# Kernel optimization log

Measured on AMD Instinct MI355X. Metric: run time of the kernel, lower is better.

## Reference

```python
import jax, jax.numpy as jnp
import numpy as np

B, T, C, NH = 4, 827, 1024, 16
HS = C // NH
SCALE = 1.0 / float(np.sqrt(HS))


def setup_inputs() -> dict:
    key = jax.random.key(0)
    ks = jax.random.split(key, 16)
    d = {}
    d["x"] = jax.random.normal(ks[0], (B, T, C), jnp.float32)
    d["x_kv"] = jax.random.normal(ks[1], (B, T, C), jnp.float32)
    d["h"] = jax.random.normal(ks[2], (B, NH, T, T), jnp.float32) * 0.1
    for i, name in enumerate(["f01", "f02", "f12", "b01", "b02", "b12"]):
        d[name] = jax.random.uniform(ks[3 + i], (B, 256, 256), jnp.float32)
    for i, name in enumerate(["Wq", "Wk", "Wv", "Wp"]):
        d[name] = jax.random.normal(ks[9 + i], (C, C), jnp.float32) * 0.02
    for name in ["bq", "bk", "bv", "bp"]:
        d[name] = jnp.zeros((C,), jnp.float32)
    return d


def _sm(a):
    return jax.nn.softmax(a, axis=-1)


def reference(x, x_kv, h, f01, f02, f12, b01, b02, b12,
              Wq, bq, Wk, bk, Wv, bv, Wp, bp):
    Bb, Tt, Cc = x.shape

    def heads(t):  # [B,T,C] -> [B,NH,T,HS]
        return t.reshape(Bb, Tt, NH, HS).transpose(0, 2, 1, 3)

    q = heads(x @ Wq.T + bq)
    k = heads(x_kv @ Wk.T + bk)
    v = heads(x_kv @ Wv.T + bv)

    att = jnp.einsum('bhqd,bhkd->bhqk', q, k) * SCALE + h  # adaptive bias add

    # region-specific partial softmax (frame1->frame0, frame2->frame0, frame2->frame1)
    att = att.at[:, :, 285:541, 0:256].set(_sm(att[:, :, 285:541, 0:256]))
    att = att.at[:, :, 571:827, 0:256].set(_sm(att[:, :, 571:827, 0:256]))
    att = att.at[:, :, 571:827, 286:542].set(_sm(att[:, :, 571:827, 286:542]))

    # bidirectional epipolar maps (backward maps used transposed)
    b01t = b01.transpose(0, 2, 1)
    b02t = b02.transpose(0, 2, 1)
    b12t = b12.transpose(0, 2, 1)
    m12 = (f12 * b12t >= 0.1).astype(att.dtype)  # [B,256,256]

    # bi_epi_ratio (T==827 branch), computed BEFORE the multiplicative masking
    r3 = att[:, :, 571:827, 286:542]            # [B,NH,256,256]
    att_mean = r3.mean(-1)                       # [B,NH,256]
    att_mask_mean = (r3 * m12[:, None]).sum(-1) / m12.sum(-1)[:, None]
    bi_epi_ratio = att_mask_mean.mean(1) / att_mean.mean(1)  # [B,256]

    # att_for: forward-only masking (clone); att: forward*backward masking
    att_for = att
    att_for = att_for.at[:, :, 285:541, 0:256].multiply(f01[:, None])
    att_for = att_for.at[:, :, 571:827, 0:256].multiply(f02[:, None])
    att_for = att_for.at[:, :, 571:827, 286:542].multiply(f12[:, None])
    att = att.at[:, :, 285:541, 0:256].multiply((b01t * f01)[:, None])
    att = att.at[:, :, 571:827, 0:256].multiply((b02t * f02)[:, None])
    att = att.at[:, :, 571:827, 286:542].multiply((b12t * f12)[:, None])

    causal = jnp.tril(jnp.ones((Tt, Tt), dtype=bool))
    aw = jnp.where(causal, att, -jnp.inf)
    # re-softmax of the already masked+multiplied regions (overwrites, then global softmax)
    aw = aw.at[:, :, 571:827, 0:256].set(_sm(att[:, :, 571:827, 0:256]))
    aw = aw.at[:, :, 571:827, 286:542].set(_sm(att[:, :, 571:827, 286:542]))
    aw = _sm(aw)

    y = jnp.einsum('bhqk,bhkd->bhqd', aw, v)
    y = y.transpose(0, 2, 1, 3).reshape(Bb, Tt, Cc)
    y = y @ Wp.T + bp  # resid dropout is identity (pdrop=0 / eval)
    return y, bi_epi_ratio
```

## Files before the change

### kernel.cpp

```cpp
#include <hip/hip_runtime.h>
#include <cstdint>
#include <cstddef>

#define Tn  827
#define Cn  1024
#define BTn 3308
#define TPn 832
#define YSZ 3387392

typedef unsigned short u16;
typedef unsigned short u16x4 __attribute__((ext_vector_type(4)));
typedef __bf16 bf16_t;
typedef bf16_t bf16x8 __attribute__((ext_vector_type(8)));
typedef float f32x4 __attribute__((ext_vector_type(4)));

#define GLD(gp, lp) __builtin_amdgcn_global_load_lds( \
    (__attribute__((address_space(1))) void*)(gp),    \
    (__attribute__((address_space(3))) void*)(lp), 16, 0, 0)

__device__ inline u16 f32_to_bf16(float f) {
  union { float f; unsigned u; } v; v.f = f;
  unsigned u = v.u;
  u += 0x7fffu + ((u >> 16) & 1u);
  return (u16)(u >> 16);
}

__global__ __launch_bounds__(256)
void cvt_all_k(const float* __restrict__ x, const float* __restrict__ xkv,
               const float* __restrict__ wq, const float* __restrict__ wk,
               const float* __restrict__ wv, const float* __restrict__ wp,
               u16* __restrict__ xb, u16* __restrict__ xkb,
               u16* __restrict__ wqb, u16* __restrict__ wkb,
               u16* __restrict__ wvb, u16* __restrict__ wpb,
               u16* __restrict__ Vt)
{
  const long NX = 846848;
  const long NW = 262144;
  long qidx = (long)blockIdx.x * 256 + threadIdx.x;
  const float* s; u16* d; long base;
  if (qidx < NX)            { s = x;   d = xb;  base = qidx; }
  else if (qidx < 2 * NX)   { s = xkv; d = xkb; base = qidx - NX; }
  else {
    long w = qidx - 2 * NX;
    int wi = (int)(w / NW);
    if (wi >= 4) {
      long p = w - 4 * NW;
      if (p < 20480) {
        int row = (int)(p / 5);
        int col = 827 + (int)(p - (long)row * 5);
        Vt[(size_t)row * TPn + col] = 0;
      }
      return;
    }
    base = w - (long)wi * NW;
    if      (wi == 0) { s = wq; d = wqb; }
    else if (wi == 1) { s = wk; d = wkb; }
    else if (wi == 2) { s = wv; d = wvb; }
    else              { s = wp; d = wpb; }
  }
  const float4 v = *(const float4*)(s + base * 4);
  u16x4 o;
  o.x = f32_to_bf16(v.x); o.y = f32_to_bf16(v.y);
  o.z = f32_to_bf16(v.z); o.w = f32_to_bf16(v.w);
  *(u16x4*)(d + base * 4) = o;
}

__global__ __launch_bounds__(256)
void gemm_qkv_k(const u16* __restrict__ xb, const u16* __restrict__ xkb,
                const u16* __restrict__ wqb, const u16* __restrict__ wkb,
                const u16* __restrict__ wvb,
                const float* __restrict__ bq, const float* __restrict__ bk,
                const float* __restrict__ bv,
                u16* __restrict__ Qb, u16* __restrict__ Kb, u16* __restrict__ Vt)
{
  const int zz = blockIdx.z;
  const u16* A  = (zz == 0) ? xb : xkb;
  const u16* Bw = (zz == 0) ? wqb : (zz == 1) ? wkb : wvb;
  const float* bias = (zz == 0) ? bq : (zz == 1) ? bk : bv;

  const int tid  = threadIdx.x;
  const int lane = tid & 63;
  const int wave = tid >> 6;
  const int wm = wave >> 1, wn = wave & 1;
  const int m0 = blockIdx.x * 128;
  const int n0 = blockIdx.y * 128;

  __shared__ u16 As[2][4096];
  __shared__ u16 Bs[2][4096];

  f32x4 acc[4][4];
  const f32x4 zero4 = {0.f, 0.f, 0.f, 0.f};
  #pragma unroll
  for (int i = 0; i < 4; ++i)
    #pragma unroll
    for (int j = 0; j < 4; ++j)
      acc[i][j] = zero4;

#define QKV_STAGE(buf_, kt_) do {                                        \
    const int k0_ = (kt_) << 5;                                          \
    _Pragma("unroll")                                                    \
    for (int it = 0; it < 2; ++it) {                                     \
      const int cbase = it * 256 + wave * 64;                            \
      const int c  = cbase + lane;                                       \
      const int r_ = c >> 2;                                             \
      const int ko_ = (c & 3) << 3;                                      \
      if (m0 + r_ < BTn)                                                 \
        GLD(A  + (size_t)(m0 + r_) * Cn + k0_ + ko_, As[buf_] + cbase * 8); \
      GLD(Bw + (size_t)(n0 + r_) * Cn + k0_ + ko_, Bs[buf_] + cbase * 8);  \
    }                                                                    \
  } while (0)

  QKV_STAGE(0, 0);
  __syncthreads();

  for (int kt = 0; kt < 32; ++kt) {
    const int cur = kt & 1;
    if (kt < 31) QKV_STAGE(cur ^ 1, kt + 1);

    bf16x8 af[4], bfr[4];
    #pragma unroll
    for (int i = 0; i < 4; ++i) {
      const int r = wm * 64 + i * 16 + (lane & 15);
      af[i] = *(const bf16x8*)(As[cur] + r * 32 + ((lane >> 4) << 3));
    }
    #pragma unroll
    for (int j = 0; j < 4; ++j) {
      const int r = wn * 64 + j * 16 + (lane & 15);
      bfr[j] = *(const bf16x8*)(Bs[cur] + r * 32 + ((lane >> 4) << 3));
    }
    #pragma unroll
    for (int i = 0; i < 4; ++i)
      #pragma unroll
      for (int j = 0; j < 4; ++j)
        acc[i][j] = __builtin_amdgcn_mfma_f32_16x16x32_bf16(af[i], bfr[j], acc[i][j], 0, 0, 0);
    __syncthreads();
  }
#undef QKV_STAGE

  const int cq = lane >> 4, cl = lane & 15;
  if (zz < 2) {
    u16* D = (zz == 0) ? Qb : Kb;
    #pragma unroll
    for (int i = 0; i < 4; ++i) {
      #pragma unroll
      for (int j = 0; j < 4; ++j) {
        const int rb  = m0 + wm * 64 + i * 16 + cq * 4;
        const int col = n0 + wn * 64 + j * 16 + cl;
        const float bc = bias[col];
        #pragma unroll
        for (int r = 0; r < 4; ++r) {
          const int row = rb + r;
          if (row < BTn) D[(size_t)row * Cn + col] = f32_to_bf16(acc[i][j][r] + bc);
        }
      }
    }
  } else {
    #pragma unroll
    for (int j = 0; j < 4; ++j) {
      const int col = n0 + wn * 64 + j * 16 + cl;
      const int hh = col >> 6, dd = col & 63;
      const float bc = bias[col];
      #pragma unroll
      for (int i = 0; i < 4; ++i) {
        const int rb = m0 + wm * 64 + i * 16 + cq * 4;
        #pragma unroll
        for (int r = 0; r < 4; ++r) {
          const int row = rb + r;
          if (row < BTn) {
            const int bb = row / Tn;
            const int t  = row - bb * Tn;
            Vt[((size_t)((bb * 16 + hh) * 64 + dd)) * TPn + t] = f32_to_bf16(acc[i][j][r] + bc);
          }
        }
      }
    }
  }
}

template<int BM, int BN, int MODE>
__global__ __launch_bounds__(256)
void gemm_k(const u16* __restrict__ Aall, const u16* __restrict__ Ball,
            const float* __restrict__ bias, float* __restrict__ Cf,
            u16* __restrict__ Cb, int M, int N, int K, int lda, int ldb, int ldc)
{
  static_assert(BM == 128, "BM fixed at 128");
  constexpr int TM = BM / 32;
  constexpr int TN = BN / 32;

  const int tid  = threadIdx.x;
  const int lane = tid & 63;
  const int wave = tid >> 6;
  const int wm = wave >> 1, wn = wave & 1;
  const int m0 = blockIdx.x * BM;
  const int n0 = blockIdx.y * BN;

  __shared__ u16 As[2][BM * 32];
  __shared__ u16 Bs[2][BN * 32];

  f32x4 acc[TM][TN];
  const f32x4 zero4 = {0.f, 0.f, 0.f, 0.f};
  #pragma unroll
  for (int i = 0; i < TM; ++i)
    #pragma unroll
    for (int j = 0; j < TN; ++j)
      acc[i][j] = zero4;

  const int nk = K >> 5;

#define OUT_STAGE(buf_, kt_) do {                                         \
    const int k0_ = (kt_) << 5;                                           \
    _Pragma("unroll")                                                     \
    for (int it = 0; it < BM / 64; ++it) {                                \
      const int cbase = it * 256 + wave * 64;                             \
      const int c  = cbase + lane;                                        \
      const int r_ = c >> 2;                                              \
      const int ko_ = (c & 3) << 3;                                       \
      if (m0 + r_ < M)                                                    \
        GLD(Aall + (size_t)(m0 + r_) * lda + k0_ + ko_, As[buf_] + cbase * 8); \
    }                                                                     \
    _Pragma("unroll")                                                     \
    for (int it = 0; it < BN / 64; ++it) {                                \
      const int cbase = it * 256 + wave * 64;                             \
      const int c  = cbase + lane;                                        \
      const int r_ = c >> 2;                                              \
      const int ko_ = (c & 3) << 3;                                       \
      if (n0 + r_ < N)                                                    \
        GLD(Ball + (size_t)(n0 + r_) * ldb + k0_ + ko_, Bs[buf_] + cbase * 8); \
    }                                                                     \
  } while (0)

  OUT_STAGE(0, 0);
  __syncthreads();

  for (int kt = 0; kt < nk; ++kt) {
    const int cur = kt & 1;
    if (kt + 1 < nk) OUT_STAGE(cur ^ 1, kt + 1);

    bf16x8 af[TM], bfr[TN];
    #pragma unroll
    for (int i = 0; i < TM; ++i) {
      const int r = wm * 64 + i * 16 + (lane & 15);
      af[i] = *(const bf16x8*)(As[cur] + r * 32 + ((lane >> 4) << 3));
    }
    #pragma unroll
    for (int j = 0; j < TN; ++j) {
      const int r = wn * (TN * 16) + j * 16 + (lane & 15);
      bfr[j] = *(const bf16x8*)(Bs[cur] + r * 32 + ((lane >> 4) << 3));
    }
    #pragma unroll
    for (int i = 0; i < TM; ++i)
      #pragma unroll
      for (int j = 0; j < TN; ++j)
        acc[i][j] = __builtin_amdgcn_mfma_f32_16x16x32_bf16(af[i], bfr[j], acc[i][j], 0, 0, 0);
    __syncthreads();
  }
#undef OUT_STAGE

  const int cq = lane >> 4, cl = lane & 15;
  #pragma unroll
  for (int i = 0; i < TM; ++i) {
    #pragma unroll
    for (int j = 0; j < TN; ++j) {
      const int rb  = m0 + wm * 64 + i * 16 + cq * 4;
      const int col = n0 + wn * (TN * 16) + j * 16 + cl;
      #pragma unroll
      for (int r = 0; r < 4; ++r) {
        const int row = rb + r;
        const float v = acc[i][j][r];
        if constexpr (MODE == 0) {
          if (row < M) Cb[(size_t)row * ldc + col] = f32_to_bf16(v + bias[col]);
        } else {
          if (row < M) Cf[(size_t)row * ldc + col] = v + bias[col];
        }
      }
    }
  }
}

__global__ __launch_bounds__(256)
void btrans_k(const float* __restrict__ b01, const float* __restrict__ b02,
              const float* __restrict__ b12, float* __restrict__ bT)
{
  const int mb = blockIdx.z;
  const int rg = mb >> 2, bb = mb & 3;
  const float* src = (rg == 0 ? b01 : rg == 1 ? b02 : b12) + (size_t)bb * 65536;
  float* dst = bT + (size_t)mb * 65536;
  const int i0 = blockIdx.x * 64, j0 = blockIdx.y * 64;
  __shared__ float tile[64 * 65];
  const int tid = threadIdx.x;
  #pragma unroll
  for (int rep = 0; rep < 16; ++rep) {
    const int idx = rep * 256 + tid;
    const int jj = idx >> 6, ii = idx & 63;
    tile[ii * 65 + jj] = src[(size_t)(j0 + jj) * 256 + i0 + ii];
  }
  __syncthreads();
  #pragma unroll
  for (int rep = 0; rep < 16; ++rep) {
    const int idx = rep * 256 + tid;
    const int ii = idx >> 6, jj = idx & 63;
    dst[(size_t)(i0 + ii) * 256 + j0 + jj] = tile[ii * 65 + jj];
  }
}

__global__ __launch_bounds__(256)
void regfused_k(const u16* __restrict__ Qb, const u16* __restrict__ Kb,
                const float* __restrict__ hsrc,
                const float* __restrict__ f01, const float* __restrict__ f02,
                const float* __restrict__ f12, const float* __restrict__ bT,
                float* __restrict__ Sreg, float* __restrict__ mmOut,
                float* __restrict__ amOut)
{
  const int zr = blockIdx.y;
  const int rg = zr % 3;
  const int z  = zr / 3;
  const int b = z >> 4, hh = z & 15;
  const int qoff = (rg == 0) ? 285 : 571;
  const int koff = (rg == 2) ? 286 : 0;
  const int m0 = blockIdx.x * 64;

  const int tid = threadIdx.x, lane = tid & 63, wave = tid >> 6;
  const int quad = lane >> 4, cl = lane & 15;

  __shared__ u16 Qs[2 * 2048];
  __shared__ u16 Ks[2 * 8192];

  const u16* qsrc = Qb + ((size_t)(b * Tn + qoff + m0)) * Cn + hh * 64;
  const u16* ksrc = Kb + ((size_t)(b * Tn + koff)) * Cn + hh * 64;
  {
    const int r  = tid >> 2;
    const int ko = (tid & 3) << 3;
    #pragma unroll
    for (int p = 0; p < 2; ++p) {
      GLD(qsrc + (size_t)r * Cn + p * 32 + ko, &Qs[p * 2048 + wave * 512]);
      #pragma unroll
      for (int it = 0; it < 4; ++it) {
        const int c  = it * 256 + tid;
        const int rr = c >> 2;
        const int kko = (c & 3) << 3;
        GLD(ksrc + (size_t)rr * Cn + p * 32 + kko,
            &Ks[p * 8192 + it * 2048 + wave * 512]);
      }
    }
  }
  __syncthreads();

  bf16x8 qa[2];
  #pragma unroll
  for (int p = 0; p < 2; ++p)
    qa[p] = *(const bf16x8*)(&Qs[p * 2048 + (wave * 16 + cl) * 32 + quad * 8]);

  f32x4 acc[16];
  const f32x4 zero4 = {0.f, 0.f, 0.f, 0.f};
  #pragma unroll
  for (int n = 0; n < 16; ++n) acc[n] = zero4;

  #pragma unroll
  for (int p = 0; p < 2; ++p)
    #pragma unroll
    for (int n = 0; n < 16; ++n) {
      const bf16x8 kb = *(const bf16x8*)(&Ks[p * 8192 + (n * 16 + cl) * 32 + quad * 8]);
      acc[n] = __builtin_amdgcn_mfma_f32_16x16x32_bf16(qa[p], kb, acc[n], 0, 0, 0);
    }

  const int i0 = m0 + wave * 16 + quad * 4;
  const float* hp = hsrc + (size_t)z * Tn * Tn + (size_t)(qoff + i0) * Tn + koff + cl;
  #pragma unroll
  for (int nb = 0; nb < 4; ++nb) {
    float hv[4][4];
    #pragma unroll
    for (int n2 = 0; n2 < 4; ++n2)
      #pragma unroll
      for (int r = 0; r < 4; ++r)
        hv[n2][r] = hp[(size_t)r * Tn + (nb * 4 + n2) * 16];
    #pragma unroll
    for (int n2 = 0; n2 < 4; ++n2)
      #pragma unroll
      for (int r = 0; r < 4; ++r)
        acc[nb * 4 + n2][r] = acc[nb * 4 + n2][r] * 0.125f + hv[n2][r];
  }

  float red[4];
  #pragma unroll
  for (int r = 0; r < 4; ++r) {
    float m = acc[0][r];
    #pragma unroll
    for (int n = 1; n < 16; ++n) m = fmaxf(m, acc[n][r]);
    m = fmaxf(m, __shfl_xor(m, 1));
    m = fmaxf(m, __shfl_xor(m, 2));
    m = fmaxf(m, __shfl_xor(m, 4));
    m = fmaxf(m, __shfl_xor(m, 8));
    red[r] = m;
  }
  #pragma unroll
  for (int n = 0; n < 16; ++n)
    #pragma unroll
    for (int r = 0; r < 4; ++r)
      acc[n][r] = __expf(acc[n][r] - red[r]);
  #pragma unroll
  for (int r = 0; r < 4; ++r) {
    float s = 0.f;
    #pragma unroll
    for (int n = 0; n < 16; ++n) s += acc[n][r];
    s += __shfl_xor(s, 1); s += __shfl_xor(s, 2);
    s += __shfl_xor(s, 4); s += __shfl_xor(s, 8);
    const float inv = 1.f / s;
    #pragma unroll
    for (int n = 0; n < 16; ++n) acc[n][r] *= inv;
  }

  const float* fp  = (rg == 0) ? f01 : (rg == 1) ? f02 : f12;
  const float* fpb = fp + ((size_t)b * 256 + i0) * 256 + cl;
  const float* bpb = bT + (((size_t)(rg * 4 + b)) << 16) + (size_t)i0 * 256 + cl;
  float msum[4] = {0.f, 0.f, 0.f, 0.f};
  float mcnt[4] = {0.f, 0.f, 0.f, 0.f};
  float asum[4] = {0.f, 0.f, 0.f, 0.f};
  #pragma unroll
  for (int nb = 0; nb < 4; ++nb) {
    float fv[4][4], bv[4][4];
    #pragma unroll
    for (int n2 = 0; n2 < 4; ++n2)
      #pragma unroll
      for (int r = 0; r < 4; ++r) {
        fv[n2][r] = fpb[(size_t)r * 256 + (nb * 4 + n2) * 16];
        bv[n2][r] = bpb[(size_t)r * 256 + (nb * 4 + n2) * 16];
      }
    #pragma unroll
    for (int n2 = 0; n2 < 4; ++n2)
      #pragma unroll
      for (int r = 0; r < 4; ++r) {
        const int n = nb * 4 + n2;
        const float prod = fv[n2][r] * bv[n2][r];
        if (rg == 2) {
          const float mk = (prod >= 0.1f) ? 1.f : 0.f;
          msum[r] += acc[n][r] * mk;
          mcnt[r] += mk;
          asum[r] += acc[n][r];
        }
        acc[n][r] *= prod;
      }
  }
  if (rg == 2) {
    #pragma unroll
    for (int r = 0; r < 4; ++r) {
      msum[r] += __shfl_xor(msum[r], 1); msum[r] += __shfl_xor(msum[r], 2);
      msum[r] += __shfl_xor(msum[r], 4); msum[r] += __shfl_xor(msum[r], 8);
      mcnt[r] += __shfl_xor(mcnt[r], 1); mcnt[r] += __shfl_xor(mcnt[r], 2);
      mcnt[r] += __shfl_xor(mcnt[r], 4); mcnt[r] += __shfl_xor(mcnt[r], 8);
      asum[r] += __shfl_xor(asum[r], 1); asum[r] += __shfl_xor(asum[r], 2);
      asum[r] += __shfl_xor(asum[r], 4); asum[r] += __shfl_xor(asum[r], 8);
    }
    if (cl == 0) {
      #pragma unroll
      for (int r = 0; r < 4; ++r) {
        const int idx = ((b * 16 + hh) << 8) + i0 + r;
        mmOut[idx] = msum[r] / mcnt[r];
        amOut[idx] = asum[r] * (1.f / 256.f);
      }
    }
  }

  if (rg != 0) {
    #pragma unroll
    for (int r = 0; r < 4; ++r) {
      float m = acc[0][r];
      #pragma unroll
      for (int n = 1; n < 16; ++n) m = fmaxf(m, acc[n][r]);
      m = fmaxf(m, __shfl_xor(m, 1));
      m = fmaxf(m, __shfl_xor(m, 2));
      m = fmaxf(m, __shfl_xor(m, 4));
      m = fmaxf(m, __shfl_xor(m, 8));
      red[r] = m;
    }
    #pragma unroll
    for (int n = 0; n < 16; ++n)
      #pragma unroll
      for (int r = 0; r < 4; ++r)
        acc[n][r] = __expf(acc[n][r] - red[r]);
    #pragma unroll
    for (int r = 0; r < 4; ++r) {
      float s = 0.f;
      #pragma unroll
      for (int n = 0; n < 16; ++n) s += acc[n][r];
      s += __shfl_xor(s, 1); s += __shfl_xor(s, 2);
      s += __shfl_xor(s, 4); s += __shfl_xor(s, 8);
      const float inv = 1.f / s;
      #pragma unroll
      for (int n = 0; n < 16; ++n) acc[n][r] *= inv;
    }
  }
  float* outp = Sreg + (((size_t)zr) << 16) + (size_t)i0 * 256 + cl;
  #pragma unroll
  for (int n = 0; n < 16; ++n)
    #pragma unroll
    for (int r = 0; r < 4; ++r)
      outp[(size_t)r * 256 + n * 16] = acc[n][r];
}

__global__ __launch_bounds__(256)
void flash_k(const u16* __restrict__ Qb, const u16* __restrict__ Kb,
             const u16* __restrict__ Vt, const float* __restrict__ hsrc,
             const float* __restrict__ Sreg, u16* __restrict__ ya)
{
  const int bid = blockIdx.x;
  const int zlow = bid & 7;
  const int t = bid >> 3;
  const int qt = t % 13;
  const int zhigh = t / 13;
  const int z = zhigh * 8 + zlow;
  const int b = z >> 4, hh = z & 15;
  const int q0 = qt * 64;

  const int tid = threadIdx.x;
  const int lane = tid & 63;
  const int wave = tid >> 6;
  const int quad = lane >> 4;
  const int cl = lane & 15;

  __shared__ u16 Qs[2][2048];
  __shared__ u16 Ks[2][2][2048];
  __shared__ u16 Vs[2][2][2048];
  __shared__ u16 Ps[4][2][512];

  {
    const u16* src = Qb + ((size_t)(b * Tn + q0)) * Cn + hh * 64;
    const int r = tid >> 2;
    const int ko = (tid & 3) << 3;
    #pragma unroll
    for (int p = 0; p < 2; ++p)
      GLD(src + (size_t)r * Cn + p * 32 + ko, &Qs[p][wave * 512]);
  }

  const u16* ksrc0 = Kb + ((size_t)(b * Tn)) * Cn + hh * 64;
  const u16* vsrc0 = Vt + ((size_t)(z * 64)) * TPn;
  const int sr  = tid >> 2;
  const int sko = (tid & 3) << 3;

#define STAGE_KV(buf_, k0_) do {                                          \
    const u16* ks_ = ksrc0 + (size_t)((k0_) + sr) * Cn;                   \
    const u16* vs_ = vsrc0 + (size_t)sr * TPn + (k0_);                    \
    _Pragma("unroll")                                                     \
    for (int p = 0; p < 2; ++p) {                                         \
      GLD(ks_ + p * 32 + sko, &Ks[buf_][p][wave * 512]);                  \
      GLD(vs_ + p * 32 + sko, &Vs[buf_][p][wave * 512]);                  \
    }                                                                     \
  } while (0)

  const int qrow_base = q0 + wave * 16 + quad * 4;
  const size_t hbase = (size_t)z * Tn * Tn;
  const float* hrow[4];
  const float* preg1[4];
  const float* preg2[4];
  int cat[4];
  #pragma unroll
  for (int r = 0; r < 4; ++r) {
    const int qq = qrow_base + r;
    const int qc = (qq < Tn) ? qq : (Tn - 1);
    hrow[r] = hsrc + hbase + (size_t)qc * Tn;
    if (qq >= 571 && qq < Tn) {
      cat[r] = 2;
      preg1[r] = Sreg + (((size_t)(z * 3 + 1)) << 16) + (size_t)(qq - 571) * 256;
      preg2[r] = Sreg + (((size_t)(z * 3 + 2)) << 16) + (size_t)(qq - 571) * 256 - 286;
    } else if (qq >= 285 && qq < 541) {
      cat[r] = 1;
      preg1[r] = Sreg + (((size_t)(z * 3 + 0)) << 16) + (size_t)(qq - 285) * 256;
      preg2[r] = hrow[r];
    } else {
      cat[r] = 0;
      preg1[r] = hrow[r];
      preg2[r] = hrow[r];
    }
  }

#define GATHER(hv_, rm_, k0_) do {                                        \
    rm_ = 0;                                                              \
    if ((k0_) < 542) {                                                    \
      _Pragma("unroll")                                                   \
      for (int j = 0; j < 4; ++j) {                                       \
        const int kk = (k0_) + j * 16 + cl;                               \
        _Pragma("unroll")                                                 \
        for (int r = 0; r < 4; ++r) {                                     \
          const float* p = hrow[r] + kk;                                  \
          bool isr = false;                                               \
          if (cat[r] == 2) {                                              \
            if (kk < 256)       { p = preg1[r] + kk; isr = true; }        \
            else if (kk >= 286 && kk < 542) { p = preg2[r] + kk; isr = true; } \
          } else if (cat[r] == 1) {                                       \
            if (kk < 256)       { p = preg1[r] + kk; isr = true; }        \
          }                                                               \
          hv_[j * 4 + r] = *p;                                            \
          if (isr) rm_ |= 1u << (j * 4 + r);                              \
        }                                                                 \
      }                                                                   \
    } else {                                                              \
      _Pragma("unroll")                                                   \
      for (int j = 0; j < 4; ++j) {                                       \
        const int kk = (k0_) + j * 16 + cl;                               \
        _Pragma("unroll")                                                 \
        for (int r = 0; r < 4; ++r) hv_[j * 4 + r] = hrow[r][kk];         \
      }                                                                   \
    }                                                                     \
  } while (0)

  STAGE_KV(0, 0);
  float hv_cur[16]; unsigned rmask_cur;
  GATHER(hv_cur, rmask_cur, 0);
  __syncthreads();

  bf16x8 qa[2];
  #pragma unroll
  for (int p = 0; p < 2; ++p)
    qa[p] = *(const bf16x8*)(&Qs[p][(wave * 16 + cl) * 32 + quad * 8]);

  f32x4 Oa[4];
  const f32x4 zero4 = {0.f, 0.f, 0.f, 0.f};
  Oa[0] = zero4; Oa[1] = zero4; Oa[2] = zero4; Oa[3] = zero4;
  float mrow[4] = {-3.0e38f, -3.0e38f, -3.0e38f, -3.0e38f};
  float lrow[4] = {0.f, 0.f, 0.f, 0.f};

  for (int kt = 0; kt <= qt; ++kt) {
    const int cur = kt & 1;
    const int k0 = kt * 64;
    const bool diag = (kt == qt);

    float hv_nxt[16]; unsigned rmask_nxt = 0;
    if (kt < qt) {
      STAGE_KV(cur ^ 1, k0 + 64);
      GATHER(hv_nxt, rmask_nxt, k0 + 64);
    }

    f32x4 sa[4];
    sa[0] = zero4; sa[1] = zero4; sa[2] = zero4; sa[3] = zero4;
    #pragma unroll
    for (int p = 0; p < 2; ++p) {
      #pragma unroll
      for (int n = 0; n < 4; ++n) {
        const bf16x8 kb = *(const bf16x8*)(&Ks[cur][p][(n * 16 + cl) * 32 + quad * 8]);
        sa[n] = __builtin_amdgcn_mfma_f32_16x16x32_bf16(qa[p], kb, sa[n], 0, 0, 0);
      }
    }

    #pragma unroll
    for (int r = 0; r < 4; ++r) {
      const int qq = qrow_base + r;
      float sv[4];
      #pragma unroll
      for (int j = 0; j < 4; ++j) {
        const int kk = k0 + j * 16 + cl;
        const float vv = ((rmask_cur >> (j * 4 + r)) & 1)
                             ? hv_cur[j * 4 + r]
                             : sa[j][r] * 0.125f + hv_cur[j * 4 + r];
        sv[j] = (diag && !(kk <= qq && qq < Tn)) ? -3.0e38f : vv;
      }
      float mx = fmaxf(fmaxf(sv[0], sv[1]), fmaxf(sv[2], sv[3]));
      mx = fmaxf(mx, __shfl_xor(mx, 1));
      mx = fmaxf(mx, __shfl_xor(mx, 2));
      mx = fmaxf(mx, __shfl_xor(mx, 4));
      mx = fmaxf(mx, __shfl_xor(mx, 8));
      const float mnew = fmaxf(mrow[r], mx);
      const float alpha = __expf(mrow[r] - mnew);
      mrow[r] = mnew;
      float ps[4], psum = 0.f;
      #pragma unroll
      for (int j = 0; j < 4; ++j) { ps[j] = __expf(sv[j] - mnew); psum += ps[j]; }
      psum += __shfl_xor(psum, 1);
      psum += __shfl_xor(psum, 2);
      psum += __shfl_xor(psum, 4);
      psum += __shfl_xor(psum, 8);
      lrow[r] = lrow[r] * alpha + psum;
      #pragma unroll
      for (int n = 0; n < 4; ++n) Oa[n][r] *= alpha;
      #pragma unroll
      for (int j = 0; j < 4; ++j)
        Ps[wave][j >> 1][(quad * 4 + r) * 32 + (j & 1) * 16 + cl] = f32_to_bf16(ps[j]);
    }

    #pragma unroll
    for (int p = 0; p < 2; ++p) {
      const bf16x8 pa = *(const bf16x8*)(&Ps[wave][p][cl * 32 + quad * 8]);
      #pragma unroll
      for (int n = 0; n < 4; ++n) {
        const bf16x8 vb = *(const bf16x8*)(&Vs[cur][p][(n * 16 + cl) * 32 + quad * 8]);
        Oa[n] = __builtin_amdgcn_mfma_f32_16x16x32_bf16(pa, vb, Oa[n], 0, 0, 0);
      }
    }

    __syncthreads();

    if (kt < qt) {
      #pragma unroll
      for (int i2 = 0; i2 < 16; ++i2) hv_cur[i2] = hv_nxt[i2];
      rmask_cur = rmask_nxt;
    }
  }
#undef STAGE_KV
#undef GATHER

  #pragma unroll
  for (int r = 0; r < 4; ++r) {
    const int qq = qrow_base + r;
    if (qq >= Tn) continue;
    const float inv = 1.f / lrow[r];
    u16* op = ya + ((size_t)(b * Tn + qq)) * Cn + hh * 64;
    #pragma unroll
    for (int n = 0; n < 4; ++n)
      op[n * 16 + cl] = f32_to_bf16(Oa[n][r] * inv);
  }
}

__global__ __launch_bounds__(256)
void ratio_k(const float* __restrict__ mm, const float* __restrict__ am,
             float* __restrict__ out)
{
  const int idx = blockIdx.x * 256 + threadIdx.x;
  const int b = idx >> 8, i = idx & 255;
  float smm = 0.f, sam = 0.f;
  #pragma unroll
  for (int hh = 0; hh < 16; ++hh) {
    smm += mm[(b * 16 + hh) * 256 + i];
    sam += am[(b * 16 + hh) * 256 + i];
  }
  out[idx] = smm / sam;
}

extern "C" void kernel_launch(void* const* d_in, const int* in_sizes, int n_in,
                              void* d_out, int out_size, void* d_ws, size_t ws_size,
                              hipStream_t stream)
{
  (void)in_sizes; (void)n_in; (void)out_size;

  const float* x   = (const float*)d_in[0];
  const float* xkv = (const float*)d_in[1];
  const float* hb  = (const float*)d_in[2];
  const float* f01 = (const float*)d_in[3];
  const float* f02 = (const float*)d_in[4];
  const float* f12 = (const float*)d_in[5];
  const float* b01 = (const float*)d_in[6];
  const float* b02 = (const float*)d_in[7];
  const float* b12 = (const float*)d_in[8];
  const float* Wq  = (const float*)d_in[9];
  const float* Wk  = (const float*)d_in[10];
  const float* Wv  = (const float*)d_in[11];
  const float* Wp  = (const float*)d_in[12];
  const float* bq  = (const float*)d_in[13];
  const float* bk  = (const float*)d_in[14];
  const float* bv  = (const float*)d_in[15];
  const float* bp  = (const float*)d_in[16];
  float* out = (float*)d_out;

  char* ws = (char*)d_ws;
  u16* xb   = (u16*)(ws + 0);
  u16* xkb  = (u16*)(ws + 6774784);
  u16* wqb  = (u16*)(ws + 13549568);
  u16* wkb  = (u16*)(ws + 15646720);
  u16* wvb  = (u16*)(ws + 17743872);
  u16* wpb  = (u16*)(ws + 19841024);
  u16* Qb   = (u16*)(ws + 21938176);
  u16* Kb   = (u16*)(ws + 28712960);
  u16* Vt   = (u16*)(ws + 42262528);
  u16* ya   = (u16*)(ws + 49078272);
  float* Sreg = (float*)(ws + 55853056);
  float* bT = (float*)(ws + 106184704);
  float* mm = (float*)(ws + 109330432);
  float* am = (float*)(ws + 109395968);
  const size_t need = 109461504;
  if (ws_size < need) return;

  cvt_all_k<<<dim3(10792), 256, 0, stream>>>(x, xkv, Wq, Wk, Wv, Wp,
                                             xb, xkb, wqb, wkb, wvb, wpb, Vt);
  btrans_k<<<dim3(4, 4, 12), 256, 0, stream>>>(b01, b02, b12, bT);
  gemm_qkv_k<<<dim3(26, 8, 3), 256, 0, stream>>>(xb, xkb, wqb, wkb, wvb,
                                                 bq, bk, bv, Qb, Kb, Vt);
  regfused_k<<<dim3(4, 192), 256, 0, stream>>>(Qb, Kb, hb, f01, f02, f12, bT,
                                               Sreg, mm, am);
  ratio_k<<<dim3(4), 256, 0, stream>>>(mm, am, out + YSZ);
  flash_k<<<dim3(832), 256, 0, stream>>>(Qb, Kb, Vt, hb, Sreg, ya);
  gemm_k<128, 64, 3><<<dim3(26, 16, 1), 256, 0, stream>>>(ya, wpb, bp, out, nullptr,
                                                          BTn, Cn, Cn, Cn, Cn, Cn);
}
```

Measured before the change: 490.4 us.

## Drop double buffering, fold softmax scale into Wq, reorder attention blocks

```diff
diff --git a/kernel.cpp b/kernel.cpp
--- a/kernel.cpp
+++ b/kernel.cpp
@@ -38,6 +38,7 @@
   const long NW = 262144;
   long qidx = (long)blockIdx.x * 256 + threadIdx.x;
   const float* s; u16* d; long base;
+  float sc = 1.0f;
   if (qidx < NX)            { s = x;   d = xb;  base = qidx; }
   else if (qidx < 2 * NX)   { s = xkv; d = xkb; base = qidx - NX; }
   else {
@@ -53,15 +54,15 @@
       return;
     }
     base = w - (long)wi * NW;
-    if      (wi == 0) { s = wq; d = wqb; }
+    if      (wi == 0) { s = wq; d = wqb; sc = 0.125f; }
     else if (wi == 1) { s = wk; d = wkb; }
     else if (wi == 2) { s = wv; d = wvb; }
     else              { s = wp; d = wpb; }
   }
   const float4 v = *(const float4*)(s + base * 4);
   u16x4 o;
-  o.x = f32_to_bf16(v.x); o.y = f32_to_bf16(v.y);
-  o.z = f32_to_bf16(v.z); o.w = f32_to_bf16(v.w);
+  o.x = f32_to_bf16(v.x * sc); o.y = f32_to_bf16(v.y * sc);
+  o.z = f32_to_bf16(v.z * sc); o.w = f32_to_bf16(v.w * sc);
   *(u16x4*)(d + base * 4) = o;
 }
 
@@ -77,6 +78,7 @@
   const u16* A  = (zz == 0) ? xb : xkb;
   const u16* Bw = (zz == 0) ? wqb : (zz == 1) ? wkb : wvb;
   const float* bias = (zz == 0) ? bq : (zz == 1) ? bk : bv;
+  const float bsc = (zz == 0) ? 0.125f : 1.0f;
 
   const int tid  = threadIdx.x;
   const int lane = tid & 63;
@@ -85,8 +87,8 @@
   const int m0 = blockIdx.x * 128;
   const int n0 = blockIdx.y * 128;
 
-  __shared__ u16 As[2][4096];
-  __shared__ u16 Bs[2][4096];
+  __shared__ u16 As[128 * 32];
+  __shared__ u16 Bs[128 * 32];
 
   f32x4 acc[4][4];
   const f32x4 zero4 = {0.f, 0.f, 0.f, 0.f};
@@ -96,46 +98,38 @@
     for (int j = 0; j < 4; ++j)
       acc[i][j] = zero4;
 
-#define QKV_STAGE(buf_, kt_) do {                                        \
-    const int k0_ = (kt_) << 5;                                          \
-    _Pragma("unroll")                                                    \
-    for (int it = 0; it < 2; ++it) {                                     \
-      const int cbase = it * 256 + wave * 64;                            \
-      const int c  = cbase + lane;                                       \
-      const int r_ = c >> 2;                                             \
-      const int ko_ = (c & 3) << 3;                                      \
-      if (m0 + r_ < BTn)                                                 \
-        GLD(A  + (size_t)(m0 + r_) * Cn + k0_ + ko_, As[buf_] + cbase * 8); \
-      GLD(Bw + (size_t)(n0 + r_) * Cn + k0_ + ko_, Bs[buf_] + cbase * 8);  \
-    }                                                                    \
-  } while (0)
-
-  QKV_STAGE(0, 0);
-  __syncthreads();
-
   for (int kt = 0; kt < 32; ++kt) {
-    const int cur = kt & 1;
-    if (kt < 31) QKV_STAGE(cur ^ 1, kt + 1);
+    const int k0 = kt << 5;
+    __syncthreads();
+    #pragma unroll
+    for (int it = 0; it < 2; ++it) {
+      const int cbase = it * 256 + wave * 64;
+      const int c  = cbase + lane;
+      const int r  = c >> 2;
+      const int ko = (c & 3) << 3;
+      if (m0 + r < BTn)
+        GLD(A  + (size_t)(m0 + r) * Cn + k0 + ko, As + cbase * 8);
+      GLD(Bw + (size_t)(n0 + r) * Cn + k0 + ko, Bs + cbase * 8);
+    }
+    __syncthreads();
 
     bf16x8 af[4], bfr[4];
     #pragma unroll
     for (int i = 0; i < 4; ++i) {
       const int r = wm * 64 + i * 16 + (lane & 15);
-      af[i] = *(const bf16x8*)(As[cur] + r * 32 + ((lane >> 4) << 3));
+      af[i] = *(const bf16x8*)(As + r * 32 + ((lane >> 4) << 3));
     }
     #pragma unroll
     for (int j = 0; j < 4; ++j) {
       const int r = wn * 64 + j * 16 + (lane & 15);
-      bfr[j] = *(const bf16x8*)(Bs[cur] + r * 32 + ((lane >> 4) << 3));
+      bfr[j] = *(const bf16x8*)(Bs + r * 32 + ((lane >> 4) << 3));
     }
     #pragma unroll
     for (int i = 0; i < 4; ++i)
       #pragma unroll
       for (int j = 0; j < 4; ++j)
         acc[i][j] = __builtin_amdgcn_mfma_f32_16x16x32_bf16(af[i], bfr[j], acc[i][j], 0, 0, 0);
-    __syncthreads();
-  }
-#undef QKV_STAGE
+  }
 
   const int cq = lane >> 4, cl = lane & 15;
   if (zz < 2) {
@@ -146,7 +140,7 @@
       for (int j = 0; j < 4; ++j) {
         const int rb  = m0 + wm * 64 + i * 16 + cq * 4;
         const int col = n0 + wn * 64 + j * 16 + cl;
-        const float bc = bias[col];
+        const float bc = bias[col] * bsc;
         #pragma unroll
         for (int r = 0; r < 4; ++r) {
           const int row = rb + r;
@@ -194,8 +188,8 @@
   const int m0 = blockIdx.x * BM;
   const int n0 = blockIdx.y * BN;
 
-  __shared__ u16 As[2][BM * 32];
-  __shared__ u16 Bs[2][BN * 32];
+  __shared__ u16 As[BM * 32];
+  __shared__ u16 Bs[BN * 32];
 
   f32x4 acc[TM][TN];
   const f32x4 zero4 = {0.f, 0.f, 0.f, 0.f};
@@ -207,54 +201,46 @@
 
   const int nk = K >> 5;
 
-#define OUT_STAGE(buf_, kt_) do {                                         \
-    const int k0_ = (kt_) << 5;                                           \
-    _Pragma("unroll")                                                     \
-    for (int it = 0; it < BM / 64; ++it) {                                \
-      const int cbase = it * 256 + wave * 64;                             \
-      const int c  = cbase + lane;                                        \
-      const int r_ = c >> 2;                                              \
-      const int ko_ = (c & 3) << 3;                                       \
-      if (m0 + r_ < M)                                                    \
-        GLD(Aall + (size_t)(m0 + r_) * lda + k0_ + ko_, As[buf_] + cbase * 8); \
-    }                                                                     \
-    _Pragma("unroll")                                                     \
-    for (int it = 0; it < BN / 64; ++it) {                                \
-      const int cbase = it * 256 + wave * 64;                             \
-      const int c  = cbase + lane;                                        \
-      const int r_ = c >> 2;                                              \
-      const int ko_ = (c & 3) << 3;                                       \
-      if (n0 + r_ < N)                                                    \
-        GLD(Ball + (size_t)(n0 + r_) * ldb + k0_ + ko_, Bs[buf_] + cbase * 8); \
-    }                                                                     \
-  } while (0)
-
-  OUT_STAGE(0, 0);
-  __syncthreads();
-
   for (int kt = 0; kt < nk; ++kt) {
-    const int cur = kt & 1;
-    if (kt + 1 < nk) OUT_STAGE(cur ^ 1, kt + 1);
+    const int k0 = kt << 5;
+    __syncthreads();
+    #pragma unroll
+    for (int it = 0; it < BM / 64; ++it) {
+      const int cbase = it * 256 + wave * 64;
+      const int c  = cbase + lane;
+      const int r  = c >> 2;
+      const int ko = (c & 3) << 3;
+      if (m0 + r < M)
+        GLD(Aall + (size_t)(m0 + r) * lda + k0 + ko, As + cbase * 8);
+    }
+    #pragma unroll
+    for (int it = 0; it < BN / 64; ++it) {
+      const int cbase = it * 256 + wave * 64;
+      const int c  = cbase + lane;
+      const int r  = c >> 2;
+      const int ko = (c & 3) << 3;
+      if (n0 + r < N)
+        GLD(Ball + (size_t)(n0 + r) * ldb + k0 + ko, Bs + cbase * 8);
+    }
+    __syncthreads();
 
     bf16x8 af[TM], bfr[TN];
     #pragma unroll
     for (int i = 0; i < TM; ++i) {
       const int r = wm * 64 + i * 16 + (lane & 15);
-      af[i] = *(const bf16x8*)(As[cur] + r * 32 + ((lane >> 4) << 3));
+      af[i] = *(const bf16x8*)(As + r * 32 + ((lane >> 4) << 3));
     }
     #pragma unroll
     for (int j = 0; j < TN; ++j) {
       const int r = wn * (TN * 16) + j * 16 + (lane & 15);
-      bfr[j] = *(const bf16x8*)(Bs[cur] + r * 32 + ((lane >> 4) << 3));
+      bfr[j] = *(const bf16x8*)(Bs + r * 32 + ((lane >> 4) << 3));
     }
     #pragma unroll
     for (int i = 0; i < TM; ++i)
       #pragma unroll
       for (int j = 0; j < TN; ++j)
         acc[i][j] = __builtin_amdgcn_mfma_f32_16x16x32_bf16(af[i], bfr[j], acc[i][j], 0, 0, 0);
-    __syncthreads();
-  }
-#undef OUT_STAGE
+  }
 
   const int cq = lane >> 4, cl = lane & 15;
   #pragma unroll
@@ -377,7 +363,7 @@
     for (int n2 = 0; n2 < 4; ++n2)
       #pragma unroll
       for (int r = 0; r < 4; ++r)
-        acc[nb * 4 + n2][r] = acc[nb * 4 + n2][r] * 0.125f + hv[n2][r];
+        acc[nb * 4 + n2][r] = acc[nb * 4 + n2][r] + hv[n2][r];
   }
 
   float red[4];
@@ -503,11 +489,9 @@
              const float* __restrict__ Sreg, u16* __restrict__ ya)
 {
   const int bid = blockIdx.x;
-  const int zlow = bid & 7;
-  const int t = bid >> 3;
-  const int qt = t % 13;
-  const int zhigh = t / 13;
-  const int z = zhigh * 8 + zlow;
+  const int g   = bid >> 6;
+  const int qt  = 12 - g;
+  const int z   = bid & 63;
   const int b = z >> 4, hh = z & 15;
   const int q0 = qt * 64;
 
@@ -517,10 +501,9 @@
   const int quad = lane >> 4;
   const int cl = lane & 15;
 
-  __shared__ u16 Qs[2][2048];
-  __shared__ u16 Ks[2][2][2048];
-  __shared__ u16 Vs[2][2][2048];
-  __shared__ u16 Ps[4][2][512];
+  __shared__ u16 Ks[2][2048];
+  __shared__ u16 Vs[2][2048];
+  __shared__ u16 QP[4096];
 
   {
     const u16* src = Qb + ((size_t)(b * Tn + q0)) * Cn + hh * 64;
@@ -528,7 +511,7 @@
     const int ko = (tid & 3) << 3;
     #pragma unroll
     for (int p = 0; p < 2; ++p)
-      GLD(src + (size_t)r * Cn + p * 32 + ko, &Qs[p][wave * 512]);
+      GLD(src + (size_t)r * Cn + p * 32 + ko, &QP[p * 2048 + wave * 512]);
   }
 
   const u16* ksrc0 = Kb + ((size_t)(b * Tn)) * Cn + hh * 64;
@@ -536,13 +519,13 @@
   const int sr  = tid >> 2;
   const int sko = (tid & 3) << 3;
 
-#define STAGE_KV(buf_, k0_) do {                                          \
+#define STAGE_KV(k0_) do {                                                \
     const u16* ks_ = ksrc0 + (size_t)((k0_) + sr) * Cn;                   \
     const u16* vs_ = vsrc0 + (size_t)sr * TPn + (k0_);                    \
     _Pragma("unroll")                                                     \
     for (int p = 0; p < 2; ++p) {                                         \
-      GLD(ks_ + p * 32 + sko, &Ks[buf_][p][wave * 512]);                  \
-      GLD(vs_ + p * 32 + sko, &Vs[buf_][p][wave * 512]);                  \
+      GLD(ks_ + p * 32 + sko, &Ks[p][wave * 512]);                        \
+      GLD(vs_ + p * 32 + sko, &Vs[p][wave * 512]);                        \
     }                                                                     \
   } while (0)
 
@@ -602,15 +585,12 @@
     }                                                                     \
   } while (0)
 
-  STAGE_KV(0, 0);
-  float hv_cur[16]; unsigned rmask_cur;
-  GATHER(hv_cur, rmask_cur, 0);
   __syncthreads();
 
   bf16x8 qa[2];
   #pragma unroll
   for (int p = 0; p < 2; ++p)
-    qa[p] = *(const bf16x8*)(&Qs[p][(wave * 16 + cl) * 32 + quad * 8]);
+    qa[p] = *(const bf16x8*)(&QP[p * 2048 + (wave * 16 + cl) * 32 + quad * 8]);
 
   f32x4 Oa[4];
   const f32x4 zero4 = {0.f, 0.f, 0.f, 0.f};
@@ -619,23 +599,26 @@
   float lrow[4] = {0.f, 0.f, 0.f, 0.f};
 
   for (int kt = 0; kt <= qt; ++kt) {
-    const int cur = kt & 1;
     const int k0 = kt * 64;
     const bool diag = (kt == qt);
 
-    float hv_nxt[16]; unsigned rmask_nxt = 0;
-    if (kt < qt) {
-      STAGE_KV(cur ^ 1, k0 + 64);
-      GATHER(hv_nxt, rmask_nxt, k0 + 64);
-    }
+    __syncthreads();
+    STAGE_KV(k0);
+    float hv[16]; unsigned rmask;
+    GATHER(hv, rmask, k0);
+    __syncthreads();
 
     f32x4 sa[4];
-    sa[0] = zero4; sa[1] = zero4; sa[2] = zero4; sa[3] = zero4;
+    #pragma unroll
+    for (int n = 0; n < 4; ++n) {
+      sa[n][0] = hv[n * 4 + 0]; sa[n][1] = hv[n * 4 + 1];
+      sa[n][2] = hv[n * 4 + 2]; sa[n][3] = hv[n * 4 + 3];
+    }
     #pragma unroll
     for (int p = 0; p < 2; ++p) {
       #pragma unroll
       for (int n = 0; n < 4; ++n) {
-        const bf16x8 kb = *(const bf16x8*)(&Ks[cur][p][(n * 16 + cl) * 32 + quad * 8]);
+        const bf16x8 kb = *(const bf16x8*)(&Ks[p][(n * 16 + cl) * 32 + quad * 8]);
         sa[n] = __builtin_amdgcn_mfma_f32_16x16x32_bf16(qa[p], kb, sa[n], 0, 0, 0);
       }
     }
@@ -647,9 +630,7 @@
       #pragma unroll
       for (int j = 0; j < 4; ++j) {
         const int kk = k0 + j * 16 + cl;
-        const float vv = ((rmask_cur >> (j * 4 + r)) & 1)
-                             ? hv_cur[j * 4 + r]
-                             : sa[j][r] * 0.125f + hv_cur[j * 4 + r];
+        const float vv = ((rmask >> (j * 4 + r)) & 1) ? hv[j * 4 + r] : sa[j][r];
         sv[j] = (diag && !(kk <= qq && qq < Tn)) ? -3.0e38f : vv;
       }
       float mx = fmaxf(fmaxf(sv[0], sv[1]), fmaxf(sv[2], sv[3]));
@@ -672,25 +653,18 @@
       for (int n = 0; n < 4; ++n) Oa[n][r] *= alpha;
       #pragma unroll
       for (int j = 0; j < 4; ++j)
-        Ps[wave][j >> 1][(quad * 4 + r) * 32 + (j & 1) * 16 + cl] = f32_to_bf16(ps[j]);
+        QP[wave * 1024 + (j >> 1) * 512 + (quad * 4 + r) * 32 + (j & 1) * 16 + cl]
+            = f32_to_bf16(ps[j]);
     }
 
     #pragma unroll
     for (int p = 0; p < 2; ++p) {
-      const bf16x8 pa = *(const bf16x8*)(&Ps[wave][p][cl * 32 + quad * 8]);
+      const bf16x8 pa = *(const bf16x8*)(&QP[wave * 1024 + p * 512 + cl * 32 + quad * 8]);
       #pragma unroll
       for (int n = 0; n < 4; ++n) {
-        const bf16x8 vb = *(const bf16x8*)(&Vs[cur][p][(n * 16 + cl) * 32 + quad * 8]);
+        const bf16x8 vb = *(const bf16x8*)(&Vs[p][(n * 16 + cl) * 32 + quad * 8]);
         Oa[n] = __builtin_amdgcn_mfma_f32_16x16x32_bf16(pa, vb, Oa[n], 0, 0, 0);
       }
-    }
-
-    __syncthreads();
-
-    if (kt < qt) {
-      #pragma unroll
-      for (int i2 = 0; i2 < 16; ++i2) hv_cur[i2] = hv_nxt[i2];
-      rmask_cur = rmask_nxt;
     }
   }
 #undef STAGE_KV
```

Measured after the change: 459.3 us. 1.07x faster.
